# Kernel tuning notes

Measured on AMD Instinct MI355X. Metric: run time of the kernel, lower is better.

Reference implementation:

```python
import jax, jax.numpy as jnp
import numpy as np

EPS = 1e-12
PERP_EPS = 1e-10


def setup_inputs() -> dict:
    key = jax.random.key(0)
    k1, k2, k3 = jax.random.split(key, 3)
    B, D, H, W = 32, 64, 32, 32
    K = 1024
    inputs = jax.random.normal(k1, (B, D, H, W), dtype=jnp.float32)
    codebooks = jax.random.normal(k2, (K, D), dtype=jnp.float32)
    noise = jax.random.normal(k3, (B * H * W, D), dtype=jnp.float32)
    return {"inputs": inputs, "codebooks": codebooks, "noise": noise}


def reference(inputs, codebooks, noise):
    B, D, H, W = inputs.shape
    K = codebooks.shape[0]
    # NCHW -> NHWC -> (N, D)
    x = jnp.transpose(inputs, (0, 2, 3, 1)).reshape(-1, D)
    distances = (
        jnp.sum(x * x, axis=1, keepdims=True)
        - 2.0 * jnp.einsum("nd,kd->nk", x, codebooks)
        + jnp.sum(codebooks * codebooks, axis=1)[None, :]
    )
    min_indices = jnp.argmin(distances, axis=1)  # (N,)
    best_entries = codebooks[min_indices]  # gather, (N, D)
    # per-row norm-matched noise injection (NSVQ)
    norm_best = jnp.sqrt(jnp.sum((x - best_entries) ** 2, axis=1, keepdims=True))
    norm_rand = jnp.sqrt(jnp.sum(noise * noise, axis=1, keepdims=True))
    vq_error = (norm_best / norm_rand + EPS) * noise
    quantized = x + vq_error
    quantized = jnp.transpose(quantized.reshape(B, H, W, D), (0, 3, 1, 2))
    # perplexity from one-hot usage histogram
    N = x.shape[0]
    counts = jnp.zeros((K,), dtype=jnp.float32).at[min_indices].add(1.0)
    avg_probs = counts / N
    perplexity = jnp.exp(-jnp.sum(avg_probs * jnp.log(avg_probs + PERP_EPS)))
    return quantized, perplexity
```

## Files before the change

kernel.cpp:

```cpp
#include <hip/hip_runtime.h>
#include <hip/hip_bf16.h>
#include <math.h>

#define BB 32
#define DD 64
#define HH 32
#define WW 32
#define NN (BB * HH * WW)
#define KK 1024
#define HW (HH * WW)
#define NQ (BB * DD * HH * WW)
#define NBLK 512

#define EPS_F 1e-12f
#define PERP_EPS_F 1e-10f
#define DIST_BIAS 512.0f

typedef __attribute__((ext_vector_type(8))) __bf16 bf16x8;
typedef __attribute__((ext_vector_type(8))) unsigned short u16x8;
typedef __attribute__((ext_vector_type(4))) float f32x4;

static __device__ __forceinline__ unsigned short f2bf(float f) {
    union { float f; unsigned int u; } c;
    c.f = f;
    unsigned int r = c.u + 0x7FFFu + ((c.u >> 16) & 1u);
    return (unsigned short)(r >> 16);
}

__global__ __launch_bounds__(256) void k_prep(const float* __restrict__ cb,
                                              unsigned short* __restrict__ cbs,
                                              float* __restrict__ cnorm,
                                              unsigned int* __restrict__ counts) {
    const int gt = blockIdx.x * 256 + threadIdx.x;
    const int j = gt >> 2;
    const int q = gt & 3;
    const int jt = j >> 4;
    const int col = j & 15;
    const float4* src = reinterpret_cast<const float4*>(cb + (size_t)j * DD + q * 16);
    float4 v0 = src[0], v1 = src[1], v2 = src[2], v3 = src[3];
    float s = v0.x * v0.x + v0.y * v0.y + v0.z * v0.z + v0.w * v0.w
            + v1.x * v1.x + v1.y * v1.y + v1.z * v1.z + v1.w * v1.w
            + v2.x * v2.x + v2.y * v2.y + v2.z * v2.z + v2.w * v2.w
            + v3.x * v3.x + v3.y * v3.y + v3.z * v3.z + v3.w * v3.w;

#pragma unroll
    for (int i2 = 0; i2 < 2; ++i2) {
        const int quad_lin = q * 2 + i2;
        const int frag = quad_lin >> 2;
        const int quad = quad_lin & 3;
        const int lane = quad * 16 + col;
        u16x8 pk;
        if (i2 == 0) {
            pk[0] = f2bf(v0.x); pk[1] = f2bf(v0.y); pk[2] = f2bf(v0.z); pk[3] = f2bf(v0.w);
            pk[4] = f2bf(v1.x); pk[5] = f2bf(v1.y); pk[6] = f2bf(v1.z); pk[7] = f2bf(v1.w);
        } else {
            pk[0] = f2bf(v2.x); pk[1] = f2bf(v2.y); pk[2] = f2bf(v2.z); pk[3] = f2bf(v2.w);
            pk[4] = f2bf(v3.x); pk[5] = f2bf(v3.y); pk[6] = f2bf(v3.z); pk[7] = f2bf(v3.w);
        }
        *reinterpret_cast<u16x8*>(cbs + ((size_t)(jt * 2 + frag) * 64 + lane) * 8) = pk;
    }

    s += __shfl_xor(s, 1);
    s += __shfl_xor(s, 2);
    if (q == 0) {
        cnorm[j] = s + DIST_BIAS;
        counts[j] = 0u;
    }
}

__global__ __launch_bounds__(512) void k_main(const float* __restrict__ inp,
                                              const unsigned short* __restrict__ cbs,
                                              const float* __restrict__ cnorm,
                                              const float* __restrict__ noise,
                                              unsigned int* __restrict__ counts,
                                              float* __restrict__ out) {
    __shared__ float xs[64 * 65];
    __shared__ __align__(16) unsigned short scratch[64 * 72];
    __shared__ unsigned int mg[64 * 4];
    __shared__ float dw[64];
    __shared__ float sxs[64];
    __shared__ float sscale[64];

    unsigned short* xls = scratch;
    unsigned short* nsu = scratch;

    const int tid = threadIdx.x;
    const int nbase = blockIdx.x * 64;
    const int b = nbase >> 10;
    const int hwbase = nbase & 1023;
    const float* xg = inp + (size_t)b * (DD * HW) + hwbase;

    const int lane = tid & 63;
    const int wid = tid >> 6;
    const int w = wid & 3;
    const int rh = wid >> 2;
    const int rbase = rh * 32;
    const int col = lane & 15;
    const int quad = lane >> 4;

    const unsigned short* bp = cbs + (size_t)w * 16 * 1024 + lane * 8;
    const float* cnp = cnorm + w * 256 + col;

    bf16x8 bb[2][4];
#pragma unroll
    for (int pg = 0; pg < 2; ++pg) {
#pragma unroll
        for (int t2 = 0; t2 < 2; ++t2) {
            const size_t off = (size_t)(pg * 2 + t2) * 1024;
            bb[pg][t2 * 2]     = *reinterpret_cast<const bf16x8*>(bp + off);
            bb[pg][t2 * 2 + 1] = *reinterpret_cast<const bf16x8*>(bp + off + 512);
        }
    }

#pragma unroll
    for (int i = 0; i < 8; ++i) {
        int idx = i * 512 + tid;
        int d = idx >> 6, r = idx & 63;
        xs[d * 65 + r] = xg[d * HW + r];
    }

    const int rrn = tid >> 3;
    const int qln = tid & 7;
    const float* nr = noise + (size_t)(nbase + rrn) * DD + qln * 8;
    const float4 nz0 = *reinterpret_cast<const float4*>(nr);
    const float4 nz1 = *reinterpret_cast<const float4*>(nr + 4);

    __syncthreads();

    {
        u16x8 pk;
        float sx = 0.0f;
#pragma unroll
        for (int j2 = 0; j2 < 8; ++j2) {
            float v = xs[(qln * 8 + j2) * 65 + rrn];
            pk[j2] = f2bf(v);
            sx = fmaf(v, v, sx);
        }
        *reinterpret_cast<u16x8*>(&xls[rrn * 72 + qln * 8]) = pk;
        sx += __shfl_xor(sx, 1); sx += __shfl_xor(sx, 2); sx += __shfl_xor(sx, 4);
        if (qln == 0) sxs[rrn] = sx;
    }
    __syncthreads();

    const bf16x8 a00 = *reinterpret_cast<const bf16x8*>(&xls[(rbase + col) * 72 + quad * 8]);
    const bf16x8 a01 = *reinterpret_cast<const bf16x8*>(&xls[(rbase + col) * 72 + 32 + quad * 8]);
    const bf16x8 a10 = *reinterpret_cast<const bf16x8*>(&xls[(rbase + 16 + col) * 72 + quad * 8]);
    const bf16x8 a11 = *reinterpret_cast<const bf16x8*>(&xls[(rbase + 16 + col) * 72 + 32 + quad * 8]);

    unsigned int minu[8];
#pragma unroll
    for (int s = 0; s < 8; ++s) minu[s] = 0xFFFFFFFFu;

#pragma unroll
    for (int g = 0; g < 8; ++g) {
        const int cb_ = g & 1;
#pragma unroll
        for (int t2 = 0; t2 < 2; ++t2) {
            const int jt = g * 2 + t2;
            f32x4 acc0 = {0.f, 0.f, 0.f, 0.f};
            f32x4 acc1 = {0.f, 0.f, 0.f, 0.f};
            acc0 = __builtin_amdgcn_mfma_f32_16x16x32_bf16(a00, bb[cb_][t2 * 2], acc0, 0, 0, 0);
            acc0 = __builtin_amdgcn_mfma_f32_16x16x32_bf16(a01, bb[cb_][t2 * 2 + 1], acc0, 0, 0, 0);
            acc1 = __builtin_amdgcn_mfma_f32_16x16x32_bf16(a10, bb[cb_][t2 * 2], acc1, 0, 0, 0);
            acc1 = __builtin_amdgcn_mfma_f32_16x16x32_bf16(a11, bb[cb_][t2 * 2 + 1], acc1, 0, 0, 0);
            const float cnt = cnp[jt * 16];
            const unsigned int jc = (unsigned int)(jt * 16 + col);
#pragma unroll
            for (int r = 0; r < 4; ++r) {
                float d0 = fmaf(-2.0f, acc0[r], cnt);
                unsigned int u0 = (__float_as_uint(d0) & ~255u) | jc;
                minu[r] = minu[r] < u0 ? minu[r] : u0;
                float d1 = fmaf(-2.0f, acc1[r], cnt);
                unsigned int u1 = (__float_as_uint(d1) & ~255u) | jc;
                minu[4 + r] = minu[4 + r] < u1 ? minu[4 + r] : u1;
            }
        }
        if (g < 6) {
#pragma unroll
            for (int t2 = 0; t2 < 2; ++t2) {
                const size_t off = (size_t)((g + 2) * 2 + t2) * 1024;
                bb[cb_][t2 * 2]     = *reinterpret_cast<const bf16x8*>(bp + off);
                bb[cb_][t2 * 2 + 1] = *reinterpret_cast<const bf16x8*>(bp + off + 512);
            }
        }
    }

#pragma unroll
    for (int s = 0; s < 8; ++s) {
        unsigned int v = minu[s];
#pragma unroll
        for (int off = 1; off < 16; off <<= 1) {
            unsigned int ov = (unsigned int)__shfl_xor((int)v, off);
            v = v < ov ? v : ov;
        }
        if (col == 0) {
            const int rloc = rbase + (s >> 2) * 16 + quad * 4 + (s & 3);
            mg[rloc * 4 + w] = v;
        }
    }
    __syncthreads();

    if (tid < 64) {
        unsigned int best = mg[tid * 4 + 0];
        unsigned int bestd = best & ~255u;
        int j = (int)(best & 255u);
#pragma unroll
        for (int q = 1; q < 4; ++q) {
            unsigned int uq = mg[tid * 4 + q];
            unsigned int dq = uq & ~255u;
            if (dq < bestd) { bestd = dq; j = q * 256 + (int)(uq & 255u); }
        }
        dw[tid] = __uint_as_float(bestd) - DIST_BIAS;
        atomicAdd(&counts[j], 1u);
    }
    __syncthreads();

    {
        float sn = 0.0f;
        sn = fmaf(nz0.x, nz0.x, sn); sn = fmaf(nz0.y, nz0.y, sn);
        sn = fmaf(nz0.z, nz0.z, sn); sn = fmaf(nz0.w, nz0.w, sn);
        sn = fmaf(nz1.x, nz1.x, sn); sn = fmaf(nz1.y, nz1.y, sn);
        sn = fmaf(nz1.z, nz1.z, sn); sn = fmaf(nz1.w, nz1.w, sn);
        sn += __shfl_xor(sn, 1); sn += __shfl_xor(sn, 2); sn += __shfl_xor(sn, 4);
        if (qln == 0) {
            float nb2 = fmaxf(dw[rrn] + sxs[rrn], 0.0f);
            sscale[rrn] = sqrtf(nb2) / sqrtf(sn) + EPS_F;
        }
        u16x8 pk;
        pk[0] = f2bf(nz0.x); pk[1] = f2bf(nz0.y); pk[2] = f2bf(nz0.z); pk[3] = f2bf(nz0.w);
        pk[4] = f2bf(nz1.x); pk[5] = f2bf(nz1.y); pk[6] = f2bf(nz1.z); pk[7] = f2bf(nz1.w);
        *reinterpret_cast<u16x8*>(&nsu[rrn * 65 + qln * 8]) = pk;
    }
    __syncthreads();

#pragma unroll
    for (int i = 0; i < 8; ++i) {
        int idx = i * 512 + tid;
        int d = idx >> 6, r = idx & 63;
        unsigned int nu = (unsigned int)nsu[r * 65 + d] << 16;
        out[(size_t)(b * DD + d) * HW + hwbase + r] =
            xs[d * 65 + r] + sscale[r] * __uint_as_float(nu);
    }
}

__global__ __launch_bounds__(1024) void k_perp(const unsigned int* __restrict__ counts,
                                               float* __restrict__ out) {
    __shared__ float red[16];
    const int tid = threadIdx.x;
    const int lane = tid & 63;
    float p = (float)counts[tid] * (1.0f / (float)NN);
    float t = p * logf(p + PERP_EPS_F);
#pragma unroll
    for (int off = 32; off > 0; off >>= 1) t += __shfl_down(t, off);
    if (lane == 0) red[tid >> 6] = t;
    __syncthreads();
    if (tid == 0) {
        float s = 0.0f;
#pragma unroll
        for (int i = 0; i < 16; ++i) s += red[i];
        out[0] = expf(-s);
    }
}

extern "C" void kernel_launch(void* const* d_in, const int* in_sizes, int n_in,
                              void* d_out, int out_size, void* d_ws, size_t ws_size,
                              hipStream_t stream) {
    (void)in_sizes; (void)n_in; (void)out_size; (void)ws_size;
    const float* inp   = (const float*)d_in[0];
    const float* cb    = (const float*)d_in[1];
    const float* noise = (const float*)d_in[2];
    float* out = (float*)d_out;

    char* ws = (char*)d_ws;
    float*          cnorm  = (float*)ws;
    unsigned int*   counts = (unsigned int*)(ws + 4096);
    unsigned short* cbs    = (unsigned short*)(ws + 8192);

    k_prep<<<16, 256, 0, stream>>>(cb, cbs, cnorm, counts);
    k_main<<<NBLK, 512, 0, stream>>>(inp, cbs, cnorm, noise, counts, out);
    k_perp<<<1, 1024, 0, stream>>>(counts, out + NQ);
}
```

Baseline: 92.43 us.

## Fuse perplexity reduction into main kernel via last-block atomic counter

Removes the separate perplexity kernel launch. Each main block increments a global done counter, and the last block to finish reads the histogram with atomic loads and computes the perplexity. The prep kernel is relaunched as 32 blocks of 128 threads and also resets the counter. The change saves one launch and its gap, at the cost of an extra atomic per block and relying on atomic ordering for the memory visibility of the counts.

```diff
diff --git a/kernel.cpp b/kernel.cpp
--- a/kernel.cpp
+++ b/kernel.cpp
@@ -27,11 +27,13 @@
     return (unsigned short)(r >> 16);
 }
 
-__global__ __launch_bounds__(256) void k_prep(const float* __restrict__ cb,
+__global__ __launch_bounds__(128) void k_prep(const float* __restrict__ cb,
                                               unsigned short* __restrict__ cbs,
                                               float* __restrict__ cnorm,
-                                              unsigned int* __restrict__ counts) {
-    const int gt = blockIdx.x * 256 + threadIdx.x;
+                                              unsigned int* __restrict__ counts,
+                                              unsigned int* __restrict__ done) {
+    const int gt = blockIdx.x * 128 + threadIdx.x;
+    if (gt == 0) done[0] = 0u;
     const int j = gt >> 2;
     const int q = gt & 3;
     const int jt = j >> 4;
@@ -73,6 +75,7 @@
                                               const float* __restrict__ cnorm,
                                               const float* __restrict__ noise,
                                               unsigned int* __restrict__ counts,
+                                              unsigned int* __restrict__ done,
                                               float* __restrict__ out) {
     __shared__ float xs[64 * 65];
     __shared__ __align__(16) unsigned short scratch[64 * 72];
@@ -80,6 +83,8 @@
     __shared__ float dw[64];
     __shared__ float sxs[64];
     __shared__ float sscale[64];
+    __shared__ float red[8];
+    __shared__ int lastflag;
 
     unsigned short* xls = scratch;
     unsigned short* nsu = scratch;
@@ -211,7 +216,8 @@
             if (dq < bestd) { bestd = dq; j = q * 256 + (int)(uq & 255u); }
         }
         dw[tid] = __uint_as_float(bestd) - DIST_BIAS;
-        atomicAdd(&counts[j], 1u);
+        unsigned int ack = atomicAdd(&counts[j], 1u);
+        ((volatile unsigned int*)mg)[tid] = ack;
     }
     __syncthreads();
 
@@ -241,24 +247,30 @@
         out[(size_t)(b * DD + d) * HW + hwbase + r] =
             xs[d * 65 + r] + sscale[r] * __uint_as_float(nu);
     }
-}
-
-__global__ __launch_bounds__(1024) void k_perp(const unsigned int* __restrict__ counts,
-                                               float* __restrict__ out) {
-    __shared__ float red[16];
-    const int tid = threadIdx.x;
-    const int lane = tid & 63;
-    float p = (float)counts[tid] * (1.0f / (float)NN);
-    float t = p * logf(p + PERP_EPS_F);
-#pragma unroll
-    for (int off = 32; off > 0; off >>= 1) t += __shfl_down(t, off);
-    if (lane == 0) red[tid >> 6] = t;
+
     __syncthreads();
     if (tid == 0) {
-        float s = 0.0f;
-#pragma unroll
-        for (int i = 0; i < 16; ++i) s += red[i];
-        out[0] = expf(-s);
+        unsigned int old = atomicAdd(done, 1u);
+        lastflag = (old == NBLK - 1) ? 1 : 0;
+    }
+    __syncthreads();
+    if (lastflag) {
+        float t = 0.0f;
+#pragma unroll
+        for (int i = 0; i < 2; ++i) {
+            unsigned int c = atomicAdd(&counts[tid + i * 512], 0u);
+            float p = (float)c * (1.0f / (float)NN);
+            t += p * logf(p + PERP_EPS_F);
+        }
+#pragma unroll
+        for (int off = 1; off < 64; off <<= 1) t += __shfl_xor(t, off);
+        if (lane == 0) red[wid] = t;
+        __syncthreads();
+        if (tid == 0) {
+            float s = red[0] + red[1] + red[2] + red[3]
+                    + red[4] + red[5] + red[6] + red[7];
+            out[NQ] = expf(-s);
+        }
     }
 }
 
@@ -274,9 +286,9 @@
     char* ws = (char*)d_ws;
     float*          cnorm  = (float*)ws;
     unsigned int*   counts = (unsigned int*)(ws + 4096);
-    unsigned short* cbs    = (unsigned short*)(ws + 8192);
-
-    k_prep<<<16, 256, 0, stream>>>(cb, cbs, cnorm, counts);
-    k_main<<<NBLK, 512, 0, stream>>>(inp, cbs, cnorm, noise, counts, out);
-    k_perp<<<1, 1024, 0, stream>>>(counts, out + NQ);
-}
+    unsigned int*   done   = (unsigned int*)(ws + 8192);
+    unsigned short* cbs    = (unsigned short*)(ws + 12288);
+
+    k_prep<<<32, 128, 0, stream>>>(cb, cbs, cnorm, counts, done);
+    k_main<<<NBLK, 512, 0, stream>>>(inp, cbs, cnorm, noise, counts, done, out);
+}
```

Result: no change. 94.00 us (+1.7%).
